# Optimization experiments

Hardware: AMD Instinct MI355X
Metric: run time of the kernel (lower is better)

The kernel has to match this reference:

```python
import jax, jax.numpy as jnp
import numpy as np

NP_, NS, EMB, HID, E, L = 100000, 10000, 256, 128, 500000, 200000


def setup_inputs() -> dict:
    key = jax.random.key(0)
    ks = jax.random.split(key, 24)
    g = lambda k, shape, fan: (jax.random.normal(k, shape, jnp.float32) / np.float32(np.sqrt(fan)))
    z = lambda n: jnp.zeros((n,), jnp.float32)
    inp = {
        "x_paper": jax.random.normal(ks[0], (NP_, EMB), jnp.float32),
        "x_software": jax.random.normal(ks[1], (NS, EMB), jnp.float32),
        "paper_id": jnp.arange(NP_, dtype=jnp.int32),
        "software_id": jnp.arange(NS, dtype=jnp.int32),
        "edge_src": jax.random.randint(ks[2], (E,), 0, NP_),
        "edge_dst": jax.random.randint(ks[3], (E,), 0, NS),
        "lbl_paper": jax.random.randint(ks[4], (L,), 0, NP_),
        "lbl_software": jax.random.randint(ks[5], (L,), 0, NS),
        # fused embedding + linear params
        "paper_emb": g(ks[6], (NP_, HID), HID),
        "software_emb": g(ks[7], (NS, HID), HID),
        "Wp": g(ks[8], (EMB, HID), EMB), "bp": z(HID),
        "Ws": g(ks[9], (EMB, HID), EMB), "bs": z(HID),
        # SAGEConv params: _ps = paper->software (dst software), _sp = software->paper
        "Wl1_ps": g(ks[10], (HID, HID), HID), "bl1_ps": z(HID), "Wr1_ps": g(ks[11], (HID, HID), HID),
        "Wl1_sp": g(ks[12], (HID, HID), HID), "bl1_sp": z(HID), "Wr1_sp": g(ks[13], (HID, HID), HID),
        "Wl2_ps": g(ks[14], (HID, HID), HID), "bl2_ps": z(HID), "Wr2_ps": g(ks[15], (HID, HID), HID),
        "Wl2_sp": g(ks[16], (HID, HID), HID), "bl2_sp": z(HID), "Wr2_sp": g(ks[17], (HID, HID), HID),
        # classifier MLP
        "Wc1": g(ks[18], (2 * HID, HID), 2 * HID), "bc1": z(HID),
        "Wc2": g(ks[19], (HID, 1), HID), "bc2": z(1),
    }
    return inp


def _sage(x_src, x_dst, src, dst, Wl, bl, Wr, n_dst):
    # PyG SAGEConv (mean aggr): lin_l(mean_j x_src[j]) + lin_r(x_dst)
    agg = jax.ops.segment_sum(x_src[src], dst, num_segments=n_dst)
    deg = jax.ops.segment_sum(jnp.ones(src.shape, x_src.dtype), dst, num_segments=n_dst)
    agg = agg / jnp.maximum(deg, 1.0)[:, None]
    return agg @ Wl + bl + x_dst @ Wr


def reference(x_paper, x_software, paper_id, software_id, edge_src, edge_dst,
              lbl_paper, lbl_software, paper_emb, software_emb, Wp, bp, Ws, bs,
              Wl1_ps, bl1_ps, Wr1_ps, Wl1_sp, bl1_sp, Wr1_sp,
              Wl2_ps, bl2_ps, Wr2_ps, Wl2_sp, bl2_sp, Wr2_sp,
              Wc1, bc1, Wc2, bc2):
    # input fusion: linear projection + id embedding (dropout in eval mode = identity)
    x_p = x_paper @ Wp + bp + paper_emb[paper_id]          # [NP, HID]
    x_s = x_software @ Ws + bs + software_emb[software_id]  # [NS, HID]
    # hetero layer 1 (each node type has one incoming edge type; aggr='sum' trivial)
    h_s = jax.nn.relu(_sage(x_p, x_s, edge_src, edge_dst, Wl1_ps, bl1_ps, Wr1_ps, NS))
    h_p = jax.nn.relu(_sage(x_s, x_p, edge_dst, edge_src, Wl1_sp, bl1_sp, Wr1_sp, NP_))
    # hetero layer 2 (no activation)
    o_s = _sage(h_p, h_s, edge_src, edge_dst, Wl2_ps, bl2_ps, Wr2_ps, NS)
    o_p = _sage(h_s, h_p, edge_dst, edge_src, Wl2_sp, bl2_sp, Wr2_sp, NP_)
    # gather-MLP edge classifier
    zc = jnp.concatenate([o_p[lbl_paper], o_s[lbl_software]], axis=-1)  # [L, 2*HID]
    h = jax.nn.relu(zc @ Wc1 + bc1)
    return (h @ Wc2 + bc2).squeeze(-1)  # [L]
```

## Files before the change

### kernel.cpp

```cpp
#include <hip/hip_runtime.h>

#define NPn 100000
#define NSn 10000
#define EMBn 256
#define HIDn 128
#define NEn 500000
#define NLn 200000

__device__ __forceinline__ void gl_lds16(const float* g, float* l) {
  __builtin_amdgcn_global_load_lds(
      (const __attribute__((address_space(1))) void*)g,
      (__attribute__((address_space(3))) void*)l, 16, 0, 0);
}

__device__ __forceinline__ float4 f4fma(float s, float4 w, float4 a) {
  a.x = fmaf(s, w.x, a.x); a.y = fmaf(s, w.y, a.y);
  a.z = fmaf(s, w.z, a.z); a.w = fmaf(s, w.w, a.w);
  return a;
}

__global__ void k_hist(const int* __restrict__ es, const int* __restrict__ ed,
                       int* __restrict__ dp, int* __restrict__ dsw) {
  const int stride = gridDim.x * blockDim.x;
  for (int i = blockIdx.x * blockDim.x + threadIdx.x; i < NEn; i += stride) {
    atomicAdd(&dp[es[i]], 1);
    atomicAdd(&dsw[ed[i]], 1);
  }
}

__global__ __launch_bounds__(1024) void k_scan1(const int* __restrict__ deg, int n,
    int* __restrict__ off, int* __restrict__ bsum) {
  __shared__ int wsum[16];
  const int t = threadIdx.x, lane = t & 63, w = t >> 6;
  const int i = blockIdx.x * 1024 + t;
  const int v = (i < n) ? deg[i] : 0;
  int x = v;
#pragma unroll
  for (int o = 1; o < 64; o <<= 1) { int y = __shfl_up(x, o); if (lane >= o) x += y; }
  if (lane == 63) wsum[w] = x;
  __syncthreads();
  if (t < 16) {
    int s = wsum[t];
#pragma unroll
    for (int o = 1; o < 16; o <<= 1) { int y = __shfl_up(s, o); if (t >= o) s += y; }
    wsum[t] = s;
  }
  __syncthreads();
  const int excl = (x - v) + (w ? wsum[w - 1] : 0);
  if (i < n) off[i] = excl;
  if (t == 1023) bsum[blockIdx.x] = excl + v;
}

__global__ __launch_bounds__(1024) void k_scan2(int* __restrict__ bsum, int nb,
    int* __restrict__ off, int n) {
  __shared__ int wsum[16];
  const int t = threadIdx.x, lane = t & 63, w = t >> 6;
  const int v = (t < nb) ? bsum[t] : 0;
  int x = v;
#pragma unroll
  for (int o = 1; o < 64; o <<= 1) { int y = __shfl_up(x, o); if (lane >= o) x += y; }
  if (lane == 63) wsum[w] = x;
  __syncthreads();
  if (t < 16) {
    int s = wsum[t];
#pragma unroll
    for (int o = 1; o < 16; o <<= 1) { int y = __shfl_up(s, o); if (t >= o) s += y; }
    wsum[t] = s;
  }
  __syncthreads();
  const int excl = (x - v) + (w ? wsum[w - 1] : 0);
  if (t < nb) bsum[t] = excl;
  if (t == nb - 1) off[n] = excl + v;
}

__global__ void k_scan3(int* __restrict__ off, int* __restrict__ cur,
                        const int* __restrict__ bsum, int n) {
  const int i = blockIdx.x * blockDim.x + threadIdx.x;
  if (i < n) {
    const int o = off[i] + bsum[i >> 10];
    off[i] = o;
    cur[i] = o;
  }
}

__global__ void k_fill(const int* __restrict__ es, const int* __restrict__ ed,
                       int* __restrict__ cur_p, int* __restrict__ cur_s,
                       int* __restrict__ csr_p, int* __restrict__ csr_s) {
  const int stride = gridDim.x * blockDim.x;
  for (int e = blockIdx.x * blockDim.x + threadIdx.x; e < NEn; e += stride) {
    const int s = es[e], d = ed[e];
    const int ps = atomicAdd(&cur_s[d], 1);
    csr_s[ps] = s;
    const int pp = atomicAdd(&cur_p[s], 1);
    csr_p[pp] = d;
  }
}

__global__ __launch_bounds__(256) void k_gather(const float* __restrict__ X,
    const int* __restrict__ off, const int* __restrict__ lst,
    float* __restrict__ agg, int n) {
  const int q = threadIdx.x & 31;
  const int g0 = (blockIdx.x * blockDim.x + threadIdx.x) >> 5;
  const int gs = (gridDim.x * blockDim.x) >> 5;
  for (int d = g0; d < n; d += gs) {
    const int s0 = off[d], s1 = off[d + 1];
    float4 a0 = make_float4(0.f, 0.f, 0.f, 0.f);
    float4 a1 = make_float4(0.f, 0.f, 0.f, 0.f);
    int e = s0;
    for (; e + 2 <= s1; e += 2) {
      const int sa = lst[e], sb = lst[e + 1];
      const float4 va = ((const float4*)X)[(size_t)sa * 32 + q];
      const float4 vb = ((const float4*)X)[(size_t)sb * 32 + q];
      a0.x += va.x; a0.y += va.y; a0.z += va.z; a0.w += va.w;
      a1.x += vb.x; a1.y += vb.y; a1.z += vb.z; a1.w += vb.w;
    }
    if (e < s1) {
      const int sa = lst[e];
      const float4 va = ((const float4*)X)[(size_t)sa * 32 + q];
      a0.x += va.x; a0.y += va.y; a0.z += va.z; a0.w += va.w;
    }
    const int dg = s1 - s0;
    const float inv = 1.0f / (float)(dg > 1 ? dg : 1);
    float4 r;
    r.x = (a0.x + a1.x) * inv; r.y = (a0.y + a1.y) * inv;
    r.z = (a0.z + a1.z) * inv; r.w = (a0.w + a1.w) * inv;
    ((float4*)agg)[(size_t)d * 32 + q] = r;
  }
}


__global__ __launch_bounds__(256) void k_input(const float* __restrict__ X,
    const float* __restrict__ W, const float* __restrict__ b,
    const float* __restrict__ emb, const int* __restrict__ ids,
    float* __restrict__ out, int M) {
  __shared__ float xs[32 * 256];
  const int t = threadIdx.x, cg = t & 31, rg = t >> 5;
  const int lane = t & 63, wv = t >> 6;
  const float4 bq = *(const float4*)(b + 4 * cg);
  const int ntiles = (M + 31) >> 5;
  for (int tile = blockIdx.x; tile < ntiles; tile += gridDim.x) {
    const int row0 = tile << 5;
#pragma unroll
    for (int r = 0; r < 8; ++r) {
      int row = row0 + wv * 8 + r;
      row = row < M ? row : M - 1;
      gl_lds16(X + (size_t)row * 256 + lane * 4, xs + (wv * 8 + r) * 256);
    }
    asm volatile("s_waitcnt vmcnt(0)" ::: "memory");
    __syncthreads();
    float4 acc0 = {0,0,0,0}, acc1 = {0,0,0,0}, acc2 = {0,0,0,0}, acc3 = {0,0,0,0};
    const float4* xr = (const float4*)(xs) + (size_t)(4 * rg) * 64;
    const float* Wc = W + 4 * cg;
#pragma unroll 4
    for (int k4 = 0; k4 < 64; ++k4) {
      const float4 w0 = *(const float4*)(Wc + (k4 * 4 + 0) * 128);
      const float4 w1 = *(const float4*)(Wc + (k4 * 4 + 1) * 128);
      const float4 w2 = *(const float4*)(Wc + (k4 * 4 + 2) * 128);
      const float4 w3 = *(const float4*)(Wc + (k4 * 4 + 3) * 128);
      const float4 x0 = xr[0 * 64 + k4], x1 = xr[1 * 64 + k4];
      const float4 x2 = xr[2 * 64 + k4], x3 = xr[3 * 64 + k4];
      acc0 = f4fma(x0.x, w0, f4fma(x0.y, w1, f4fma(x0.z, w2, f4fma(x0.w, w3, acc0))));
      acc1 = f4fma(x1.x, w0, f4fma(x1.y, w1, f4fma(x1.z, w2, f4fma(x1.w, w3, acc1))));
      acc2 = f4fma(x2.x, w0, f4fma(x2.y, w1, f4fma(x2.z, w2, f4fma(x2.w, w3, acc2))));
      acc3 = f4fma(x3.x, w0, f4fma(x3.y, w1, f4fma(x3.z, w2, f4fma(x3.w, w3, acc3))));
    }
    __syncthreads();
    float4 accs[4] = {acc0, acc1, acc2, acc3};
#pragma unroll
    for (int i = 0; i < 4; ++i) {
      const int row = row0 + 4 * rg + i;
      if (row < M) {
        const float4 eq = *(const float4*)(emb + (size_t)ids[row] * 128 + 4 * cg);
        float4 v = accs[i];
        v.x += bq.x + eq.x; v.y += bq.y + eq.y;
        v.z += bq.z + eq.z; v.w += bq.w + eq.w;
        *(float4*)(out + (size_t)row * 128 + 4 * cg) = v;
      }
    }
  }
}

__global__ __launch_bounds__(256) void k_sage(const float* __restrict__ AGG,
    const float* __restrict__ Xd, const float* __restrict__ Wl,
    const float* __restrict__ Wr, const float* __restrict__ b,
    float* __restrict__ out, int M, int dorelu) {
  __shared__ float xs[32 * 256];
  const int t = threadIdx.x, cg = t & 31, rg = t >> 5;
  const int lane = t & 63, wv = t >> 6;
  const float4 bq = *(const float4*)(b + 4 * cg);
  const int ntiles = (M + 31) >> 5;
  for (int tile = blockIdx.x; tile < ntiles; tile += gridDim.x) {
    const int row0 = tile << 5;
#pragma unroll
    for (int r = 0; r < 8; ++r) {
      int row = row0 + wv * 8 + r;
      row = row < M ? row : M - 1;
      const float* src = (lane < 32)
          ? AGG + (size_t)row * 128 + lane * 4
          : Xd + (size_t)row * 128 + (lane - 32) * 4;
      gl_lds16(src, xs + (wv * 8 + r) * 256);
    }
    asm volatile("s_waitcnt vmcnt(0)" ::: "memory");
    __syncthreads();
    float4 acc0 = {0,0,0,0}, acc1 = {0,0,0,0}, acc2 = {0,0,0,0}, acc3 = {0,0,0,0};
    const float4* xr = (const float4*)(xs) + (size_t)(4 * rg) * 64;
    const float* Wlc = Wl + 4 * cg;
    const float* Wrc = Wr + 4 * cg;
#pragma unroll 4
    for (int k4 = 0; k4 < 32; ++k4) {
      const float4 w0 = *(const float4*)(Wlc + (k4 * 4 + 0) * 128);
      const float4 w1 = *(const float4*)(Wlc + (k4 * 4 + 1) * 128);
      const float4 w2 = *(const float4*)(Wlc + (k4 * 4 + 2) * 128);
      const float4 w3 = *(const float4*)(Wlc + (k4 * 4 + 3) * 128);
      const float4 x0 = xr[0 * 64 + k4], x1 = xr[1 * 64 + k4];
      const float4 x2 = xr[2 * 64 + k4], x3 = xr[3 * 64 + k4];
      acc0 = f4fma(x0.x, w0, f4fma(x0.y, w1, f4fma(x0.z, w2, f4fma(x0.w, w3, acc0))));
      acc1 = f4fma(x1.x, w0, f4fma(x1.y, w1, f4fma(x1.z, w2, f4fma(x1.w, w3, acc1))));
      acc2 = f4fma(x2.x, w0, f4fma(x2.y, w1, f4fma(x2.z, w2, f4fma(x2.w, w3, acc2))));
      acc3 = f4fma(x3.x, w0, f4fma(x3.y, w1, f4fma(x3.z, w2, f4fma(x3.w, w3, acc3))));
    }
#pragma unroll 4
    for (int k4 = 32; k4 < 64; ++k4) {
      const float4 w0 = *(const float4*)(Wrc + ((k4 - 32) * 4 + 0) * 128);
      const float4 w1 = *(const float4*)(Wrc + ((k4 - 32) * 4 + 1) * 128);
      const float4 w2 = *(const float4*)(Wrc + ((k4 - 32) * 4 + 2) * 128);
      const float4 w3 = *(const float4*)(Wrc + ((k4 - 32) * 4 + 3) * 128);
      const float4 x0 = xr[0 * 64 + k4], x1 = xr[1 * 64 + k4];
      const float4 x2 = xr[2 * 64 + k4], x3 = xr[3 * 64 + k4];
      acc0 = f4fma(x0.x, w0, f4fma(x0.y, w1, f4fma(x0.z, w2, f4fma(x0.w, w3, acc0))));
      acc1 = f4fma(x1.x, w0, f4fma(x1.y, w1, f4fma(x1.z, w2, f4fma(x1.w, w3, acc1))));
      acc2 = f4fma(x2.x, w0, f4fma(x2.y, w1, f4fma(x2.z, w2, f4fma(x2.w, w3, acc2))));
      acc3 = f4fma(x3.x, w0, f4fma(x3.y, w1, f4fma(x3.z, w2, f4fma(x3.w, w3, acc3))));
    }
    __syncthreads();
    float4 accs[4] = {acc0, acc1, acc2, acc3};
#pragma unroll
    for (int i = 0; i < 4; ++i) {
      const int row = row0 + 4 * rg + i;
      if (row < M) {
        float4 v = accs[i];
        v.x += bq.x; v.y += bq.y; v.z += bq.z; v.w += bq.w;
        if (dorelu) {
          v.x = fmaxf(v.x, 0.f); v.y = fmaxf(v.y, 0.f);
          v.z = fmaxf(v.z, 0.f); v.w = fmaxf(v.w, 0.f);
        }
        *(float4*)(out + (size_t)row * 128 + 4 * cg) = v;
      }
    }
  }
}

__global__ __launch_bounds__(256) void k_cls(const float* __restrict__ OP,
    const float* __restrict__ OS, const int* __restrict__ LP,
    const int* __restrict__ LS, const float* __restrict__ W,
    const float* __restrict__ b1, const float* __restrict__ W2,
    const float* __restrict__ b2, float* __restrict__ out, int M) {
  __shared__ float xs[32 * 256];
  const int t = threadIdx.x, cg = t & 31, rg = t >> 5;
  const int lane = t & 63, wv = t >> 6;
  const float4 b1q = *(const float4*)(b1 + 4 * cg);
  const float4 w2q = *(const float4*)(W2 + 4 * cg);
  const float b2v = b2[0];
  const int ntiles = (M + 31) >> 5;
  for (int tile = blockIdx.x; tile < ntiles; tile += gridDim.x) {
    const int row0 = tile << 5;
#pragma unroll
    for (int r = 0; r < 8; ++r) {
      int row = row0 + wv * 8 + r;
      row = row < M ? row : M - 1;
      const float* src = (lane < 32)
          ? OP + (size_t)LP[row] * 128 + lane * 4
          : OS + (size_t)LS[row] * 128 + (lane - 32) * 4;
      gl_lds16(src, xs + (wv * 8 + r) * 256);
    }
    asm volatile("s_waitcnt vmcnt(0)" ::: "memory");
    __syncthreads();
    float4 acc0 = {0,0,0,0}, acc1 = {0,0,0,0}, acc2 = {0,0,0,0}, acc3 = {0,0,0,0};
    const float4* xr = (const float4*)(xs) + (size_t)(4 * rg) * 64;
    const float* Wc = W + 4 * cg;
#pragma unroll 4
    for (int k4 = 0; k4 < 64; ++k4) {
      const float4 w0 = *(const float4*)(Wc + (k4 * 4 + 0) * 128);
      const float4 w1 = *(const float4*)(Wc + (k4 * 4 + 1) * 128);
      const float4 w2 = *(const float4*)(Wc + (k4 * 4 + 2) * 128);
      const float4 w3 = *(const float4*)(Wc + (k4 * 4 + 3) * 128);
      const float4 x0 = xr[0 * 64 + k4], x1 = xr[1 * 64 + k4];
      const float4 x2 = xr[2 * 64 + k4], x3 = xr[3 * 64 + k4];
      acc0 = f4fma(x0.x, w0, f4fma(x0.y, w1, f4fma(x0.z, w2, f4fma(x0.w, w3, acc0))));
      acc1 = f4fma(x1.x, w0, f4fma(x1.y, w1, f4fma(x1.z, w2, f4fma(x1.w, w3, acc1))));
      acc2 = f4fma(x2.x, w0, f4fma(x2.y, w1, f4fma(x2.z, w2, f4fma(x2.w, w3, acc2))));
      acc3 = f4fma(x3.x, w0, f4fma(x3.y, w1, f4fma(x3.z, w2, f4fma(x3.w, w3, acc3))));
    }
    __syncthreads();
    float4 accs[4] = {acc0, acc1, acc2, acc3};
#pragma unroll
    for (int i = 0; i < 4; ++i) {
      float4 h = accs[i];
      float v = fmaxf(h.x + b1q.x, 0.f) * w2q.x + fmaxf(h.y + b1q.y, 0.f) * w2q.y +
                fmaxf(h.z + b1q.z, 0.f) * w2q.z + fmaxf(h.w + b1q.w, 0.f) * w2q.w;
#pragma unroll
      for (int o = 16; o >= 1; o >>= 1) v += __shfl_xor(v, o);
      const int row = row0 + 4 * rg + i;
      if (cg == 0 && row < M) out[row] = v + b2v;
    }
  }
}

extern "C" void kernel_launch(void* const* d_in, const int* in_sizes, int n_in,
                              void* d_out, int out_size, void* d_ws, size_t ws_size,
                              hipStream_t stream) {
  const float* x_paper     = (const float*)d_in[0];
  const float* x_software  = (const float*)d_in[1];
  const int*   paper_id    = (const int*)d_in[2];
  const int*   software_id = (const int*)d_in[3];
  const int*   edge_src    = (const int*)d_in[4];
  const int*   edge_dst    = (const int*)d_in[5];
  const int*   lbl_paper   = (const int*)d_in[6];
  const int*   lbl_soft    = (const int*)d_in[7];
  const float* paper_emb   = (const float*)d_in[8];
  const float* soft_emb    = (const float*)d_in[9];
  const float* Wp = (const float*)d_in[10]; const float* bp = (const float*)d_in[11];
  const float* Ws = (const float*)d_in[12]; const float* bs = (const float*)d_in[13];
  const float* Wl1_ps = (const float*)d_in[14]; const float* bl1_ps = (const float*)d_in[15];
  const float* Wr1_ps = (const float*)d_in[16];
  const float* Wl1_sp = (const float*)d_in[17]; const float* bl1_sp = (const float*)d_in[18];
  const float* Wr1_sp = (const float*)d_in[19];
  const float* Wl2_ps = (const float*)d_in[20]; const float* bl2_ps = (const float*)d_in[21];
  const float* Wr2_ps = (const float*)d_in[22];
  const float* Wl2_sp = (const float*)d_in[23]; const float* bl2_sp = (const float*)d_in[24];
  const float* Wr2_sp = (const float*)d_in[25];
  const float* Wc1 = (const float*)d_in[26]; const float* bc1 = (const float*)d_in[27];
  const float* Wc2 = (const float*)d_in[28]; const float* bc2 = (const float*)d_in[29];
  float* outp = (float*)d_out;

  float* ws    = (float*)d_ws;
  float* x_p   = ws;
  float* x_s   = ws + 12800000;
  float* h_p   = ws + 14080000;
  float* h_s   = ws + 26880000;
  float* agg_p = ws + 28160000;
  float* agg_s = ws + 40960000;
  int*   deg_p = (int*)(ws + 42240000);
  int*   deg_s = deg_p + 100000;
  int*   off_p = deg_s + 10000;
  int*   off_s = off_p + 100001;
  int*   bsum  = off_s + 10001;
  int*   csr_p = bsum + 1024;
  int*   csr_s = csr_p + 500000;
  float* o_p = x_p;
  float* o_s = x_s;

  hipMemsetAsync(deg_p, 0, (size_t)110000 * 4, stream);
  k_hist<<<1024, 256, 0, stream>>>(edge_src, edge_dst, deg_p, deg_s);
  k_scan1<<<98, 1024, 0, stream>>>(deg_p, NPn, off_p, bsum);
  k_scan2<<<1, 1024, 0, stream>>>(bsum, 98, off_p, NPn);
  k_scan3<<<391, 256, 0, stream>>>(off_p, deg_p, bsum, NPn);
  k_scan1<<<10, 1024, 0, stream>>>(deg_s, NSn, off_s, bsum);
  k_scan2<<<1, 1024, 0, stream>>>(bsum, 10, off_s, NSn);
  k_scan3<<<40, 256, 0, stream>>>(off_s, deg_s, bsum, NSn);
  k_fill<<<1024, 256, 0, stream>>>(edge_src, edge_dst, deg_p, deg_s, csr_p, csr_s);

  k_input<<<1024, 256, 0, stream>>>(x_paper, Wp, bp, paper_emb, paper_id, x_p, NPn);
  k_input<<<313, 256, 0, stream>>>(x_software, Ws, bs, soft_emb, software_id, x_s, NSn);

  k_gather<<<1250, 256, 0, stream>>>(x_p, off_s, csr_s, agg_s, NSn);
  k_gather<<<4096, 256, 0, stream>>>(x_s, off_p, csr_p, agg_p, NPn);
  k_sage<<<313, 256, 0, stream>>>(agg_s, x_s, Wl1_ps, Wr1_ps, bl1_ps, h_s, NSn, 1);
  k_sage<<<1024, 256, 0, stream>>>(agg_p, x_p, Wl1_sp, Wr1_sp, bl1_sp, h_p, NPn, 1);

  k_gather<<<1250, 256, 0, stream>>>(h_p, off_s, csr_s, agg_s, NSn);
  k_gather<<<4096, 256, 0, stream>>>(h_s, off_p, csr_p, agg_p, NPn);
  k_sage<<<313, 256, 0, stream>>>(agg_s, h_s, Wl2_ps, Wr2_ps, bl2_ps, o_s, NSn, 0);
  k_sage<<<1024, 256, 0, stream>>>(agg_p, h_p, Wl2_sp, Wr2_sp, bl2_sp, o_p, NPn, 0);

  k_cls<<<1024, 256, 0, stream>>>(o_p, o_s, lbl_paper, lbl_soft, Wc1, bc1, Wc2, bc2,
                                  outp, NLn);
}
```

Baseline: 1.175 ms.

## Fold classifier first layer into layer-2 SAGE weights, simplify classifier

Precomputes the products of the layer-2 SAGE weight matrices and biases with the two halves of Wc1, so the layer-2 SAGE kernels directly output per-node classifier projections. The classifier then only gathers two 128-wide projections per label edge, adds them with bc1, applies ReLU and dots with Wc2. This removes the 200k x 256 x 128 GEMM in the classifier and adds a small weight-composition kernel. Floating-point rounding changes slightly because the matmuls are reassociated.

```diff
diff --git a/kernel.cpp b/kernel.cpp
--- a/kernel.cpp
+++ b/kernel.cpp
@@ -93,6 +93,37 @@
     csr_s[ps] = s;
     const int pp = atomicAdd(&cur_p[s], 1);
     csr_p[pp] = d;
+  }
+}
+
+__global__ __launch_bounds__(256) void k_wcomp(
+    const float* __restrict__ Wl_sp, const float* __restrict__ Wr_sp,
+    const float* __restrict__ Wl_ps, const float* __restrict__ Wr_ps,
+    const float* __restrict__ bl_sp, const float* __restrict__ bl_ps,
+    const float* __restrict__ Wc1,
+    float* __restrict__ Wlp, float* __restrict__ Wrp,
+    float* __restrict__ Wls, float* __restrict__ Wrs,
+    float* __restrict__ bpc, float* __restrict__ bsc) {
+  const int comp = blockIdx.x / 65, sub = blockIdx.x % 65;
+  const float* A; const float* B; float* C; const float* bin; float* bout;
+  switch (comp) {
+    case 0:  A = Wl_sp; B = Wc1;         C = Wlp; bin = bl_sp;  bout = bpc; break;
+    case 1:  A = Wr_sp; B = Wc1;         C = Wrp; bin = nullptr; bout = nullptr; break;
+    case 2:  A = Wl_ps; B = Wc1 + 16384; C = Wls; bin = bl_ps;  bout = bsc; break;
+    default: A = Wr_ps; B = Wc1 + 16384; C = Wrs; bin = nullptr; bout = nullptr; break;
+  }
+  const int t = threadIdx.x;
+  if (sub < 64) {
+    const int idx = sub * 256 + t, r = idx >> 7, c = idx & 127;
+    float acc = 0.f;
+#pragma unroll 8
+    for (int k = 0; k < 128; ++k) acc = fmaf(A[r * 128 + k], B[k * 128 + c], acc);
+    C[idx] = acc;
+  } else if (bin != nullptr && t < 128) {
+    float acc = 0.f;
+#pragma unroll 8
+    for (int k = 0; k < 128; ++k) acc = fmaf(bin[k], B[k * 128 + t], acc);
+    bout[t] = acc;
   }
 }
 
@@ -250,59 +281,27 @@
   }
 }
 
-__global__ __launch_bounds__(256) void k_cls(const float* __restrict__ OP,
-    const float* __restrict__ OS, const int* __restrict__ LP,
-    const int* __restrict__ LS, const float* __restrict__ W,
-    const float* __restrict__ b1, const float* __restrict__ W2,
-    const float* __restrict__ b2, float* __restrict__ out, int M) {
-  __shared__ float xs[32 * 256];
-  const int t = threadIdx.x, cg = t & 31, rg = t >> 5;
-  const int lane = t & 63, wv = t >> 6;
-  const float4 b1q = *(const float4*)(b1 + 4 * cg);
-  const float4 w2q = *(const float4*)(W2 + 4 * cg);
+__global__ __launch_bounds__(256) void k_cls2(const float* __restrict__ PP,
+    const float* __restrict__ PS, const int* __restrict__ LP,
+    const int* __restrict__ LS, const float* __restrict__ b1,
+    const float* __restrict__ W2, const float* __restrict__ b2,
+    float* __restrict__ out, int M) {
+  const int t = threadIdx.x, q = t & 31;
+  const int g0 = (blockIdx.x * blockDim.x + t) >> 5;
+  const int gs = (gridDim.x * blockDim.x) >> 5;
+  const float4 b1q = *(const float4*)(b1 + 4 * q);
+  const float4 w2q = *(const float4*)(W2 + 4 * q);
   const float b2v = b2[0];
-  const int ntiles = (M + 31) >> 5;
-  for (int tile = blockIdx.x; tile < ntiles; tile += gridDim.x) {
-    const int row0 = tile << 5;
-#pragma unroll
-    for (int r = 0; r < 8; ++r) {
-      int row = row0 + wv * 8 + r;
-      row = row < M ? row : M - 1;
-      const float* src = (lane < 32)
-          ? OP + (size_t)LP[row] * 128 + lane * 4
-          : OS + (size_t)LS[row] * 128 + (lane - 32) * 4;
-      gl_lds16(src, xs + (wv * 8 + r) * 256);
-    }
-    asm volatile("s_waitcnt vmcnt(0)" ::: "memory");
-    __syncthreads();
-    float4 acc0 = {0,0,0,0}, acc1 = {0,0,0,0}, acc2 = {0,0,0,0}, acc3 = {0,0,0,0};
-    const float4* xr = (const float4*)(xs) + (size_t)(4 * rg) * 64;
-    const float* Wc = W + 4 * cg;
-#pragma unroll 4
-    for (int k4 = 0; k4 < 64; ++k4) {
-      const float4 w0 = *(const float4*)(Wc + (k4 * 4 + 0) * 128);
-      const float4 w1 = *(const float4*)(Wc + (k4 * 4 + 1) * 128);
-      const float4 w2 = *(const float4*)(Wc + (k4 * 4 + 2) * 128);
-      const float4 w3 = *(const float4*)(Wc + (k4 * 4 + 3) * 128);
-      const float4 x0 = xr[0 * 64 + k4], x1 = xr[1 * 64 + k4];
-      const float4 x2 = xr[2 * 64 + k4], x3 = xr[3 * 64 + k4];
-      acc0 = f4fma(x0.x, w0, f4fma(x0.y, w1, f4fma(x0.z, w2, f4fma(x0.w, w3, acc0))));
-      acc1 = f4fma(x1.x, w0, f4fma(x1.y, w1, f4fma(x1.z, w2, f4fma(x1.w, w3, acc1))));
-      acc2 = f4fma(x2.x, w0, f4fma(x2.y, w1, f4fma(x2.z, w2, f4fma(x2.w, w3, acc2))));
-      acc3 = f4fma(x3.x, w0, f4fma(x3.y, w1, f4fma(x3.z, w2, f4fma(x3.w, w3, acc3))));
-    }
-    __syncthreads();
-    float4 accs[4] = {acc0, acc1, acc2, acc3};
-#pragma unroll
-    for (int i = 0; i < 4; ++i) {
-      float4 h = accs[i];
-      float v = fmaxf(h.x + b1q.x, 0.f) * w2q.x + fmaxf(h.y + b1q.y, 0.f) * w2q.y +
-                fmaxf(h.z + b1q.z, 0.f) * w2q.z + fmaxf(h.w + b1q.w, 0.f) * w2q.w;
-#pragma unroll
-      for (int o = 16; o >= 1; o >>= 1) v += __shfl_xor(v, o);
-      const int row = row0 + 4 * rg + i;
-      if (cg == 0 && row < M) out[row] = v + b2v;
-    }
+  for (int l = g0; l < M; l += gs) {
+    const float4 pp = *(const float4*)(PP + (size_t)LP[l] * 128 + 4 * q);
+    const float4 ps = *(const float4*)(PS + (size_t)LS[l] * 128 + 4 * q);
+    float v = fmaxf(pp.x + ps.x + b1q.x, 0.f) * w2q.x
+            + fmaxf(pp.y + ps.y + b1q.y, 0.f) * w2q.y
+            + fmaxf(pp.z + ps.z + b1q.z, 0.f) * w2q.z
+            + fmaxf(pp.w + ps.w + b1q.w, 0.f) * w2q.w;
+#pragma unroll
+    for (int o = 16; o >= 1; o >>= 1) v += __shfl_xor(v, o);
+    if (q == 0) out[l] = v + b2v;
   }
 }
 
@@ -347,8 +346,17 @@
   int*   bsum  = off_s + 10001;
   int*   csr_p = bsum + 1024;
   int*   csr_s = csr_p + 500000;
-  float* o_p = x_p;
-  float* o_s = x_s;
+  float* Wlp = (float*)(csr_s + 500000);
+  float* Wrp = Wlp + 16384;
+  float* Wls = Wrp + 16384;
+  float* Wrs = Wls + 16384;
+  float* bpc = Wrs + 16384;
+  float* bsc = bpc + 128;
+  float* proj_p = x_p;
+  float* proj_s = x_s;
+
+  k_wcomp<<<260, 256, 0, stream>>>(Wl2_sp, Wr2_sp, Wl2_ps, Wr2_ps, bl2_sp, bl2_ps,
+                                   Wc1, Wlp, Wrp, Wls, Wrs, bpc, bsc);
 
   hipMemsetAsync(deg_p, 0, (size_t)110000 * 4, stream);
   k_hist<<<1024, 256, 0, stream>>>(edge_src, edge_dst, deg_p, deg_s);
@@ -370,9 +378,9 @@
 
   k_gather<<<1250, 256, 0, stream>>>(h_p, off_s, csr_s, agg_s, NSn);
   k_gather<<<4096, 256, 0, stream>>>(h_s, off_p, csr_p, agg_p, NPn);
-  k_sage<<<313, 256, 0, stream>>>(agg_s, h_s, Wl2_ps, Wr2_ps, bl2_ps, o_s, NSn, 0);
-  k_sage<<<1024, 256, 0, stream>>>(agg_p, h_p, Wl2_sp, Wr2_sp, bl2_sp, o_p, NPn, 0);
-
-  k_cls<<<1024, 256, 0, stream>>>(o_p, o_s, lbl_paper, lbl_soft, Wc1, bc1, Wc2, bc2,
-                                  outp, NLn);
-}
+  k_sage<<<313, 256, 0, stream>>>(agg_s, h_s, Wls, Wrs, bsc, proj_s, NSn, 0);
+  k_sage<<<1024, 256, 0, stream>>>(agg_p, h_p, Wlp, Wrp, bpc, proj_p, NPn, 0);
+
+  k_cls2<<<2048, 256, 0, stream>>>(proj_p, proj_s, lbl_paper, lbl_soft, bc1, Wc2, bc2,
+                                   outp, NLn);
+}
```

Measured after the change: 974.2 us. 17.1% less time.
